# Performance work log

Measured on AMD Instinct MI355X. Metric: run time of the kernel, lower is better.

Reference implementation:

```python
import jax, jax.numpy as jnp
import numpy as np
from jax import lax

HID = 96              # hidden_dim (C)
DM  = 2 * HID         # SS2D d_model (real+imag interleaved channels)
DI  = 2 * DM          # d_inner (expand=2, VMamba default)
N   = 16              # d_state
K   = 4               # scan directions
R   = (DM + 15) // 16 # dt_rank = ceil(d_model/16)
B_, H_, W_ = 1, 64, 64


def _layernorm(x, w, b, eps=1e-5):
    m = x.mean(-1, keepdims=True)
    v = ((x - m) ** 2).mean(-1, keepdims=True)
    return (x - m) * lax.rsqrt(v + eps) * w + b


def _selective_scan(xs, delta, A, Bs, Cs):
    # xs, delta: (B,K,D,L); A: (K,D,N); Bs, Cs: (B,K,N,L)
    def step(h, inp):
        dt, Bt, Ct, ut = inp                              # (B,K,D),(B,K,N),(B,K,N),(B,K,D)
        dA = jnp.exp(dt[..., None] * A[None])             # (B,K,D,N)
        h = h * dA + dt[..., None] * Bt[:, :, None, :] * ut[..., None]
        y = jnp.einsum('bkdn,bkn->bkd', h, Ct)
        return h, y
    inputs = (jnp.moveaxis(delta, -1, 0), jnp.moveaxis(Bs, -1, 0),
              jnp.moveaxis(Cs, -1, 0), jnp.moveaxis(xs, -1, 0))
    h0 = jnp.zeros(xs.shape[:3] + (N,), xs.dtype)
    _, ys = lax.scan(step, h0, inputs)                    # (L,B,K,D)
    return jnp.moveaxis(ys, 0, -1)                        # (B,K,D,L)


def _forward_core(x, x_proj_w, dt_w, dt_b, A_logs, Ds):
    # x: (B, DI, H, W) -- 4-direction cross-scan (VMamba SS2D)
    B, D, H, W = x.shape
    L = H * W
    x_hw = x.reshape(B, D, L)
    x_wh = x.transpose(0, 1, 3, 2).reshape(B, D, L)
    x_hwwh = jnp.stack([x_hw, x_wh], axis=1)                    # (B,2,D,L)
    xs = jnp.concatenate([x_hwwh, jnp.flip(x_hwwh, -1)], 1)     # (B,4,D,L)
    x_dbl = jnp.einsum('bkdl,kcd->bkcl', xs, x_proj_w)          # (B,K,R+2N,L)
    dts, Bs, Cs = jnp.split(x_dbl, [R, R + N], axis=2)
    dts = jnp.einsum('bkrl,kdr->bkdl', dts, dt_w)
    delta = jax.nn.softplus(dts + dt_b[None, :, :, None])
    A = -jnp.exp(A_logs.reshape(K, D, N))
    ys = _selective_scan(xs, delta, A, Bs, Cs)
    out_y = ys + Ds.reshape(K, D)[None, :, :, None] * xs        # (B,4,D,L)
    inv_y = jnp.flip(out_y[:, 2:4], -1)
    tr = lambda t: t.reshape(B, D, W, H).transpose(0, 1, 3, 2).reshape(B, D, L)
    y = out_y[:, 0] + inv_y[:, 0] + tr(out_y[:, 1]) + tr(inv_y[:, 1])
    return y.transpose(0, 2, 1).reshape(B, H, W, D)


def _ss2d(x, in_proj_w, conv_w, conv_b, x_proj_w, dt_w, dt_b,
          A_logs, Ds, out_norm_w, out_norm_b, out_proj_w):
    # x: (B, H, Wf, DM)
    xz = x @ in_proj_w.T                                        # (B,H,Wf,2*DI)
    xc, z = jnp.split(xz, 2, axis=-1)
    xc = xc.transpose(0, 3, 1, 2)                               # (B,DI,H,Wf)
    xc = lax.conv_general_dilated(xc, conv_w, (1, 1), 'SAME',
                                  feature_group_count=DI,
                                  dimension_numbers=('NCHW', 'OIHW', 'NCHW'))
    xc = jax.nn.silu(xc + conv_b[None, :, None, None])
    y = _forward_core(xc, x_proj_w, dt_w, dt_b, A_logs, Ds)     # (B,H,Wf,DI)
    y = _layernorm(y, out_norm_w, out_norm_b)
    y = y * jax.nn.silu(z)
    return y @ out_proj_w.T                                     # (B,H,Wf,DM)


def _freq_vss(x, in_proj_w, conv_w, conv_b, x_proj_w, dt_w, dt_b,
              A_logs, Ds, out_norm_w, out_norm_b, out_proj_w):
    B, H, W, C = x.shape
    xf = jnp.fft.rfft2(x, axes=(1, 2), norm='ortho')            # (B,H,Wf,C) complex
    Wf = xf.shape[2]
    # interleave real/imag into channels: (B,H,Wf,C,2) -> (B,H,Wf,2C)
    x1 = jnp.stack([xf.real, xf.imag], axis=4).reshape(B, H, Wf, 2 * C)
    att = _ss2d(x1, in_proj_w, conv_w, conv_b, x_proj_w, dt_w, dt_b,
                A_logs, Ds, out_norm_w, out_norm_b, out_proj_w)
    att = att.reshape(B, H, Wf, C, 2)
    attc = lax.complex(att[..., 0], att[..., 1])
    x1r = jnp.fft.irfft2(attc, s=(H, W), axes=(1, 2), norm='ortho')
    return x + x1r                                              # residual (drop_path=0)


def setup_inputs() -> dict:
    key = jax.random.key(0)
    ks = jax.random.split(key, 8)
    s = 0.02
    return {
        'x': jax.random.normal(ks[0], (B_, H_, W_, HID), jnp.float32),
        'in_proj_w': jax.random.normal(ks[1], (2 * DI, DM), jnp.float32) * s,
        'conv_w': jax.random.normal(ks[2], (DI, 1, 3, 3), jnp.float32) * s,
        'conv_b': jnp.zeros((DI,), jnp.float32),
        'x_proj_w': jax.random.normal(ks[3], (K, R + 2 * N, DI), jnp.float32) * s,
        'dt_w': jax.random.normal(ks[4], (K, DI, R), jnp.float32) * s,
        'dt_b': jax.random.normal(ks[5], (K, DI), jnp.float32) * 0.1,
        'A_logs': jnp.tile(jnp.log(jnp.arange(1, N + 1, dtype=jnp.float32))[None], (K * DI, 1)),
        'Ds': jnp.ones((K * DI,), jnp.float32),
        'out_norm_w': jnp.ones((DI,), jnp.float32),
        'out_norm_b': jnp.zeros((DI,), jnp.float32),
        'out_proj_w': jax.random.normal(ks[6], (DM, DI), jnp.float32) * s,
    }


def reference(x, in_proj_w, conv_w, conv_b, x_proj_w, dt_w, dt_b,
              A_logs, Ds, out_norm_w, out_norm_b, out_proj_w):
    return _freq_vss(x, in_proj_w, conv_w, conv_b, x_proj_w, dt_w, dt_b,
                     A_logs, Ds, out_norm_w, out_norm_b, out_proj_w)
```

## Files before the change

kernel.cpp:

```cpp
#include <hip/hip_runtime.h>
#include <hip/hip_bf16.h>

#define LQ   2112
#define DQ   384
#define NST  16
#define HQ   64
#define WFQ  33
#define CQ   96
#define SC   66
#define KDN  24576

#define AIPW  0
#define ACW   147456
#define ACB   150912
#define AXPW  151296
#define ADTW  218880
#define ADTB  237312
#define AANEG 238848
#define ADS   263424
#define ANW   264960
#define ANB   265344
#define AOPW  265728
#define ARTOT 339456

#define OFF_FFT   339456
#define OFF_XZ    744960
#define OFF_XCV   2366976
#define OFF_G     3177984
#define OFF_SUMDT 3549696
#define OFF_HEND  3651072
#define OFF_YS    5273088
#define OFF_YS4   6084096

#define P_ZR  0
#define P_ZI  202752

static __device__ __forceinline__ float u2f(unsigned short u)
{ union { unsigned int i; float f; } v; v.i = ((unsigned int)u) << 16; return v.f; }

static __device__ __forceinline__ float ldin(const void* p, int o, int isbf)
{
    if (isbf) return u2f(((const unsigned short*)p)[o]);
    return ((const float*)p)[o];
}

static __device__ __forceinline__ int isbf_of(const void* ds)
{ return (((const unsigned int*)ds)[0] == 0x3F803F80u) ? 1 : 0; }

__global__ __launch_bounds__(256) void k_cvt_rfftw(
    const void* __restrict__ x,   const void* __restrict__ ipw,
    const void* __restrict__ cw,  const void* __restrict__ cb,
    const void* __restrict__ xpw, const void* __restrict__ dtw,
    const void* __restrict__ dtb, const void* __restrict__ alog,
    const void* __restrict__ ds,  const void* __restrict__ nw,
    const void* __restrict__ nb,  const void* __restrict__ opw,
    float* __restrict__ arena, float* __restrict__ Zr, float* __restrict__ Zi)
{
    const int isbf = isbf_of(ds);
    if (blockIdx.x < 1326) {
        int t = blockIdx.x * 256 + threadIdx.x;
        int o = t;
        if (o < 147456) { arena[t] = ldin(ipw, o, isbf); return; }  o -= 147456;
        if (o < 3456)   { arena[t] = ldin(cw, o, isbf);  return; }  o -= 3456;
        if (o < 384)    { arena[t] = ldin(cb, o, isbf);  return; }  o -= 384;
        if (o < 67584)  { arena[t] = ldin(xpw, o, isbf); return; }  o -= 67584;
        if (o < 18432)  { arena[t] = ldin(dtw, o, isbf); return; }  o -= 18432;
        if (o < 1536)   { arena[t] = ldin(dtb, o, isbf); return; }  o -= 1536;
        if (o < 24576)  { arena[t] = -expf(ldin(alog, o, isbf)); return; }  o -= 24576;
        if (o < 1536)   { arena[t] = ldin(ds, o, isbf);  return; }  o -= 1536;
        if (o < 384)    { arena[t] = ldin(nw, o, isbf);  return; }  o -= 384;
        if (o < 384)    { arena[t] = ldin(nb, o, isbf);  return; }  o -= 384;
        arena[t] = ldin(opw, o, isbf);
        return;
    }
    __shared__ float tc[64], ts[64];
    if (threadIdx.x < 64) {
        float ang = -6.283185307179586f * (float)threadIdx.x / 64.f;
        float s, c; __sincosf(ang, &s, &c); tc[threadIdx.x] = c; ts[threadIdx.x] = s;
    }
    __syncthreads();
    int tid = (blockIdx.x - 1326) * 256 + threadIdx.x;
    int c = tid % CQ; int f = (tid / CQ) % WFQ; int h = tid / (CQ * WFQ);
    const int base = h * 64 * CQ + c;
    float zr = 0.f, zi = 0.f; int j = 0;
#pragma unroll 4
    for (int w = 0; w < 64; w++) {
        float xv = ldin(x, base + w * CQ, isbf);
        zr += xv * tc[j]; zi += xv * ts[j];
        j += f; j &= 63;
    }
    Zr[tid] = zr; Zi[tid] = zi;
}

__global__ __launch_bounds__(256) void k_ffth(const float* __restrict__ Zr, const float* __restrict__ Zi,
                                              float* __restrict__ x1)
{
    __shared__ float tc[64], ts[64];
    if (threadIdx.x < 64) {
        float ang = -6.283185307179586f * (float)threadIdx.x / 64.f;
        float s, c; __sincosf(ang, &s, &c); tc[threadIdx.x] = c; ts[threadIdx.x] = s;
    }
    __syncthreads();
    int tid = blockIdx.x * 256 + threadIdx.x;
    int c = tid % CQ; int f = (tid / CQ) % WFQ; int u = tid / (CQ * WFQ);
    float xr = 0.f, xi = 0.f; int j = 0;
    int base = f * CQ + c;
#pragma unroll 4
    for (int h = 0; h < 64; h++) {
        float zr = Zr[base + h * (WFQ * CQ)];
        float zi = Zi[base + h * (WFQ * CQ)];
        xr += zr * tc[j] - zi * ts[j];
        xi += zr * ts[j] + zi * tc[j];
        j += u; j &= 63;
    }
    int l = u * WFQ + f;
    x1[l * 192 + 2 * c]     = xr * (1.f / 64.f);
    x1[l * 192 + 2 * c + 1] = xi * (1.f / 64.f);
}

typedef __attribute__((ext_vector_type(8))) __bf16 bf16x8;
typedef __attribute__((ext_vector_type(4))) float f32x4;

__global__ __launch_bounds__(256) void k_gemm(const float* __restrict__ A, const float* __restrict__ W,
                                              float* __restrict__ C, int N, int K, int sW, int sC)
{
    W += (size_t)blockIdx.z * sW; C += (size_t)blockIdx.z * sC;
    __shared__ __bf16 Asm[64 * 40];
    __shared__ __bf16 Bsm[64 * 40];
    const int tid = threadIdx.x;
    const int bm = blockIdx.y * 64, bn = blockIdx.x * 64;
    const int wv = tid >> 6, lane = tid & 63;
    const int srow = tid >> 2, skk = (tid & 3) * 8;
    const int fm = lane & 15, fq = lane >> 4;
    f32x4 acc0 = {0.f, 0.f, 0.f, 0.f}, acc1 = acc0, acc2 = acc0, acc3 = acc0;
    const __bf16* afp = Asm + (wv * 16 + fm) * 40 + fq * 8;
    const __bf16* bfp = Bsm + fm * 40 + fq * 8;
    for (int k0 = 0; k0 < K; k0 += 32) {
        {
            const float* ap = A + (size_t)(bm + srow) * K + k0 + skk;
            float4 a0 = *(const float4*)ap, a1 = *(const float4*)(ap + 4);
            bf16x8 v = { (__bf16)a0.x, (__bf16)a0.y, (__bf16)a0.z, (__bf16)a0.w,
                         (__bf16)a1.x, (__bf16)a1.y, (__bf16)a1.z, (__bf16)a1.w };
            *(bf16x8*)(Asm + srow * 40 + skk) = v;
        }
        {
            float4 b0 = {0.f,0.f,0.f,0.f}, b1 = b0;
            if (bn + srow < N) {
                const float* wp = W + (size_t)(bn + srow) * K + k0 + skk;
                b0 = *(const float4*)wp; b1 = *(const float4*)(wp + 4);
            }
            bf16x8 v = { (__bf16)b0.x, (__bf16)b0.y, (__bf16)b0.z, (__bf16)b0.w,
                         (__bf16)b1.x, (__bf16)b1.y, (__bf16)b1.z, (__bf16)b1.w };
            *(bf16x8*)(Bsm + srow * 40 + skk) = v;
        }
        __syncthreads();
        bf16x8 af = *(const bf16x8*)afp;
        bf16x8 fb0 = *(const bf16x8*)(bfp);
        bf16x8 fb1 = *(const bf16x8*)(bfp + 16 * 40);
        bf16x8 fb2 = *(const bf16x8*)(bfp + 32 * 40);
        bf16x8 fb3 = *(const bf16x8*)(bfp + 48 * 40);
        acc0 = __builtin_amdgcn_mfma_f32_16x16x32_bf16(af, fb0, acc0, 0, 0, 0);
        acc1 = __builtin_amdgcn_mfma_f32_16x16x32_bf16(af, fb1, acc1, 0, 0, 0);
        acc2 = __builtin_amdgcn_mfma_f32_16x16x32_bf16(af, fb2, acc2, 0, 0, 0);
        acc3 = __builtin_amdgcn_mfma_f32_16x16x32_bf16(af, fb3, acc3, 0, 0, 0);
        __syncthreads();
    }
    const int m0 = bm + wv * 16 + fq * 4;
#pragma unroll
    for (int nt = 0; nt < 4; nt++) {
        f32x4 a = (nt == 0) ? acc0 : ((nt == 1) ? acc1 : ((nt == 2) ? acc2 : acc3));
        int n = bn + nt * 16 + fm;
        if (n < N) {
#pragma unroll
            for (int r = 0; r < 4; r++)
                C[(size_t)(m0 + r) * N + n] = a[r];
        }
    }
}

__global__ __launch_bounds__(256) void k_conv(const float* __restrict__ xz,
                                              const float* __restrict__ ar,
                                              float* __restrict__ xcv)
{
    int tid = blockIdx.x * 256 + threadIdx.x;
    int d = tid % DQ; int lp = tid / DQ;
    int l0 = lp * 2;
    float w9[9];
#pragma unroll
    for (int i = 0; i < 9; i++) w9[i] = ar[ACW + d * 9 + i];
    float cb = ar[ACB + d];
#pragma unroll
    for (int q = 0; q < 2; q++) {
        int l = l0 + q;
        int h = l / WFQ; int f = l % WFQ;
        float acc = cb;
#pragma unroll
        for (int ky = 0; ky < 3; ky++) {
            int hh = h + ky - 1;
            if (hh < 0 || hh >= HQ) continue;
#pragma unroll
            for (int kx = 0; kx < 3; kx++) {
                int ff = f + kx - 1;
                if (ff < 0 || ff >= WFQ) continue;
                acc += w9[ky * 3 + kx] * xz[(size_t)(hh * WFQ + ff) * 768 + d];
            }
        }
        float sig = 1.f / (1.f + __expf(-acc));
        xcv[(size_t)l * DQ + d] = acc * sig;
    }
}

static __device__ __forceinline__ float softplus_f(float a)
{
    return (a > 15.f) ? a : __logf(1.f + __expf(a));
}

template<int KK> static __device__ __forceinline__ int chunk_l0(int s)
{
    if (KK == 0) return s * 32;
    if (KK == 1) return (s & 1) * 1056 + (s >> 1);
    if (KK == 2) return 2111 - s * 32;
    return 2111 - (s & 1) * 1056 - (s >> 1);
}
template<int KK> static __device__ __forceinline__ int chunk_stp()
{
    if (KK == 0) return 1;
    if (KK == 1) return 33;
    if (KK == 2) return -1;
    return -33;
}

template<int KK, int PASS2> static __device__ __forceinline__ void scan_body(
    const float* __restrict__ xcv, const float* __restrict__ G, const float* __restrict__ ar,
    float* __restrict__ hend, float* __restrict__ sumdt, float* __restrict__ ys4,
    float* __restrict__ dtL, float* __restrict__ duL,
    float* __restrict__ bvL, float* __restrict__ cvL)
{
    const int s = blockIdx.x, db = blockIdx.y;
    const int lane = threadIdx.x;
    const int d = lane & 15, ng = lane >> 4;
    const int stp = chunk_stp<KK>();
    const int l0 = chunk_l0<KK>(s);
    const float* Gk = G + (size_t)KK * (LQ * 44);

    {
        const int st = lane & 31;
        const int hi = lane >> 5;
        const int jb = hi * 8;
        const int lt = l0 + stp * st;
        const float* gr = Gk + lt * 44;
        float4 g0 = *(const float4*)(gr);
        float4 g1 = *(const float4*)(gr + 4);
        float4 g2 = *(const float4*)(gr + 8);
        float4 b0 = *(const float4*)(gr + 12 + jb);
        float4 b1 = *(const float4*)(gr + 16 + jb);
        *(float4*)(bvL + st * 20 + jb)     = b0;
        *(float4*)(bvL + st * 20 + jb + 4) = b1;
        if (PASS2) {
            float4 c0 = *(const float4*)(gr + 28 + jb);
            float4 c1 = *(const float4*)(gr + 32 + jb);
            *(float4*)(cvL + st * 20 + jb)     = c0;
            *(float4*)(cvL + st * 20 + jb + 4) = c1;
        }
        const float* ub = xcv + (size_t)lt * DQ + db * 16 + jb;
        float uu[8];
        *(float4*)(uu)     = *(const float4*)(ub);
        *(float4*)(uu + 4) = *(const float4*)(ub + 4);
#pragma unroll
        for (int j = 0; j < 8; j++) {
            const int kdj = KK * DQ + db * 16 + jb + j;
            const float* wp = ar + ADTW + kdj * 12;
            float acc = ar[ADTB + kdj]
                + wp[0] * g0.x + wp[1] * g0.y + wp[2]  * g0.z + wp[3]  * g0.w
                + wp[4] * g1.x + wp[5] * g1.y + wp[6]  * g1.z + wp[7]  * g1.w
                + wp[8] * g2.x + wp[9] * g2.y + wp[10] * g2.z + wp[11] * g2.w;
            float dtv = softplus_f(acc);
            dtL[st * 17 + jb + j] = dtv;
            duL[st * 17 + jb + j] = dtv * uu[j];
        }
    }
    __syncthreads();

    const int kd = KK * DQ + db * 16 + d;
    const int kdn = kd * NST + 4 * ng;
    const float4 Av = *(const float4*)(ar + AANEG + kdn);
    float h0 = 0.f, h1 = 0.f, h2 = 0.f, h3 = 0.f;
    if (PASS2) {
        float4 hh = *(const float4*)(hend + (size_t)s * KDN + kdn);
        h0 = hh.x; h1 = hh.y; h2 = hh.z; h3 = hh.w;
    }

    float sd_acc = 0.f;
#pragma unroll 8
    for (int i = 0; i < 32; i++) {
        float dt = dtL[i * 17 + d];
        float du = duL[i * 17 + d];
        float4 bv = *(const float4*)(bvL + i * 20 + 4 * ng);
        h0 = h0 * __expf(dt * Av.x) + du * bv.x;
        h1 = h1 * __expf(dt * Av.y) + du * bv.y;
        h2 = h2 * __expf(dt * Av.z) + du * bv.z;
        h3 = h3 * __expf(dt * Av.w) + du * bv.w;
        if (PASS2) {
            float4 cv = *(const float4*)(cvL + i * 20 + 4 * ng);
            float yp = h0 * cv.x + h1 * cv.y + h2 * cv.z + h3 * cv.w;
            yp += __shfl_xor(yp, 16);
            yp += __shfl_xor(yp, 32);
            if (ng == 0) duL[i * 17 + d] = yp;
        } else {
            sd_acc += dt;
        }
    }

    if (!PASS2) {
        *(float4*)(hend + (size_t)s * KDN + kdn) = make_float4(h0, h1, h2, h3);
        float sd = sd_acc;
        sd += __shfl_xor(sd, 16);
        sd += __shfl_xor(sd, 32);
        if (ng == 0) sumdt[s * 1536 + kd] = sd;
    } else {
        __syncthreads();
        float* ysk = ys4 + (size_t)KK * (LQ * DQ);
        const int sd16 = lane & 15, sg = lane >> 4;
#pragma unroll
        for (int e = 0; e < 8; e++) {
            const int step = e * 4 + sg;
            const int wl = l0 + stp * step;
            ysk[(size_t)wl * DQ + db * 16 + sd16] = duL[step * 17 + sd16];
        }
    }
}

__global__ __launch_bounds__(64, 4) void k_scan1(const float* __restrict__ xcv, const float* __restrict__ G,
                                                 const float* __restrict__ ar,
                                                 float* __restrict__ hend, float* __restrict__ sumdt,
                                                 float* __restrict__ ys4)
{
    __shared__ float smem[1728];
    float* dtL = smem; float* duL = smem + 544; float* bvL = smem + 1088;
    switch (blockIdx.z) {
        case 0: scan_body<0, 0>(xcv, G, ar, hend, sumdt, ys4, dtL, duL, bvL, nullptr); break;
        case 1: scan_body<1, 0>(xcv, G, ar, hend, sumdt, ys4, dtL, duL, bvL, nullptr); break;
        case 2: scan_body<2, 0>(xcv, G, ar, hend, sumdt, ys4, dtL, duL, bvL, nullptr); break;
        default: scan_body<3, 0>(xcv, G, ar, hend, sumdt, ys4, dtL, duL, bvL, nullptr); break;
    }
}

__global__ __launch_bounds__(64, 4) void k_scan2(const float* __restrict__ xcv, const float* __restrict__ G,
                                                 const float* __restrict__ ar,
                                                 float* __restrict__ hend, float* __restrict__ sumdt,
                                                 float* __restrict__ ys4)
{
    __shared__ float smem[2368];
    float* dtL = smem; float* duL = smem + 544; float* bvL = smem + 1088;
    float* cvL = smem + 1728;
    switch (blockIdx.z) {
        case 0: scan_body<0, 1>(xcv, G, ar, hend, sumdt, ys4, dtL, duL, bvL, cvL); break;
        case 1: scan_body<1, 1>(xcv, G, ar, hend, sumdt, ys4, dtL, duL, bvL, cvL); break;
        case 2: scan_body<2, 1>(xcv, G, ar, hend, sumdt, ys4, dtL, duL, bvL, cvL); break;
        default: scan_body<3, 1>(xcv, G, ar, hend, sumdt, ys4, dtL, duL, bvL, cvL); break;
    }
}

__global__ __launch_bounds__(256) void k_comb(const float* __restrict__ ar, const float* __restrict__ sumdt,
                                              float* __restrict__ hend)
{
    int tid = blockIdx.x * 256 + threadIdx.x;
    int kd = tid >> 4;
    float Av = ar[AANEG + tid];
    float hbuf[6], sbuf[6];
#pragma unroll
    for (int q = 0; q < 6; q++) {
        hbuf[q] = hend[(size_t)q * KDN + tid];
        sbuf[q] = sumdt[q * 1536 + kd];
    }
    float hp = 0.f;
    for (int s = 0; s < SC; s += 6) {
        float hc[6], sc6[6];
#pragma unroll
        for (int q = 0; q < 6; q++) { hc[q] = hbuf[q]; sc6[q] = sbuf[q]; }
#pragma unroll
        for (int q = 0; q < 6; q++) {
            int sn = s + 6 + q;
            if (sn < SC) {
                hbuf[q] = hend[(size_t)sn * KDN + tid];
                sbuf[q] = sumdt[sn * 1536 + kd];
            }
        }
#pragma unroll
        for (int q = 0; q < 6; q++) {
            hend[(size_t)(s + q) * KDN + tid] = hp;
            hp = hp * __expf(Av * sc6[q]) + hc[q];
        }
    }
}

__global__ __launch_bounds__(128) void k_lnmul(const float* __restrict__ ys4, const float* __restrict__ xcv,
                                               const float* __restrict__ xz, const float* __restrict__ ar,
                                               float* __restrict__ ym)
{
    int l = blockIdx.x; int tid = threadIdx.x;
    float v[3]; float s1 = 0.f, s2 = 0.f;
#pragma unroll
    for (int j = 0; j < 3; j++) {
        int d = tid + j * 128;
        size_t idx = (size_t)l * DQ + d;
        float sd = ar[ADS + d] + ar[ADS + DQ + d] + ar[ADS + 2 * DQ + d] + ar[ADS + 3 * DQ + d];
        float a = ys4[idx] + ys4[811008 + idx] + ys4[1622016 + idx] + ys4[2433024 + idx]
                + sd * xcv[idx];
        v[j] = a; s1 += a; s2 += a * a;
    }
#pragma unroll
    for (int off = 1; off < 64; off <<= 1) { s1 += __shfl_xor(s1, off); s2 += __shfl_xor(s2, off); }
    __shared__ float sh[4];
    if ((tid & 63) == 0) { sh[(tid >> 6) * 2] = s1; sh[(tid >> 6) * 2 + 1] = s2; }
    __syncthreads();
    s1 = sh[0] + sh[2]; s2 = sh[1] + sh[3];
    float m = s1 * (1.f / 384.f);
    float var = s2 * (1.f / 384.f) - m * m;
    float rs = rsqrtf(var + 1e-5f);
#pragma unroll
    for (int j = 0; j < 3; j++) {
        int d = tid + j * 128;
        float z = xz[(size_t)l * 768 + 384 + d];
        float sig = 1.f / (1.f + __expf(-z));
        ym[(size_t)l * DQ + d] = ((v[j] - m) * rs * ar[ANW + d] + ar[ANB + d]) * (z * sig);
    }
}

__global__ __launch_bounds__(256) void k_iffth(const float* __restrict__ att,
                                               float* __restrict__ Yr, float* __restrict__ Yi)
{
    __shared__ float tc[64], ts[64];
    if (threadIdx.x < 64) {
        float ang = 6.283185307179586f * (float)threadIdx.x / 64.f;
        float s, c; __sincosf(ang, &s, &c); tc[threadIdx.x] = c; ts[threadIdx.x] = s;
    }
    __syncthreads();
    int tid = blockIdx.x * 256 + threadIdx.x;
    int c = tid % CQ; int f = (tid / CQ) % WFQ; int hp = tid / (CQ * WFQ);
    float yr = 0.f, yi = 0.f; int j = 0;
#pragma unroll 4
    for (int h = 0; h < 64; h++) {
        const float* ap = att + (size_t)(h * WFQ + f) * 192 + 2 * c;
        float arv = ap[0], aiv = ap[1];
        yr += arv * tc[j] - aiv * ts[j];
        yi += arv * ts[j] + aiv * tc[j];
        j += hp; j &= 63;
    }
    Yr[tid] = yr * 0.125f;
    Yi[tid] = yi * 0.125f;
}

__global__ __launch_bounds__(256) void k_irfft_res(const float* __restrict__ Yr, const float* __restrict__ Yi,
                                                   const void* __restrict__ x, const void* __restrict__ ds,
                                                   void* __restrict__ out)
{
    __shared__ float tc[64], ts[64];
    if (threadIdx.x < 64) {
        float ang = 6.283185307179586f * (float)threadIdx.x / 64.f;
        float s, c; __sincosf(ang, &s, &c); tc[threadIdx.x] = c; ts[threadIdx.x] = s;
    }
    __syncthreads();
    const int isbf = isbf_of(ds);
    int tid = blockIdx.x * 256 + threadIdx.x;
    int c = tid % CQ; int w = (tid / CQ) % 64; int h = tid / (CQ * 64);
    const float* yr = Yr + h * (WFQ * CQ) + c;
    const float* yi = Yi + h * (WFQ * CQ) + c;
    float acc = yr[0];
    acc += ((w & 1) ? -1.f : 1.f) * yr[32 * CQ];
    float a2 = 0.f; int j = w & 63;
#pragma unroll 4
    for (int f = 1; f < 32; f++) {
        a2 += yr[f * CQ] * tc[j] - yi[f * CQ] * ts[j];
        j += w; j &= 63;
    }
    acc += 2.f * a2;
    float val = ldin(x, tid, isbf) + 0.125f * acc;
    if (isbf) ((__hip_bfloat16*)out)[tid] = __float2bfloat16(val);
    else      ((float*)out)[tid] = val;
}

extern "C" void kernel_launch(void* const* d_in, const int* in_sizes, int n_in,
                              void* d_out, int out_size, void* d_ws, size_t ws_size,
                              hipStream_t stream)
{
    float* ws    = (float*)d_ws;
    float* ar    = ws;
    float* Zr    = ws + OFF_FFT + P_ZR;
    float* Zi    = ws + OFF_FFT + P_ZI;
    float* xz    = ws + OFF_XZ;
    float* xcv   = ws + OFF_XCV;
    float* G     = ws + OFF_G;
    float* sumdt = ws + OFF_SUMDT;
    float* hend  = ws + OFF_HEND;
    float* x1    = ws + OFF_YS;
    float* ys4   = ws + OFF_YS4;

    float* ym   = hend;
    float* att  = xcv;

    k_cvt_rfftw<<<2118, 256, 0, stream>>>(d_in[0], d_in[1], d_in[2], d_in[3], d_in[4], d_in[5],
                                          d_in[6], d_in[7], d_in[8], d_in[9], d_in[10], d_in[11],
                                          ar, Zr, Zi);
    k_ffth<<<792, 256, 0, stream>>>(Zr, Zi, x1);
    k_gemm<<<dim3(12, 33, 1), 256, 0, stream>>>(x1, ar + AIPW, xz, 768, 192, 0, 0);
    k_conv<<<1584, 256, 0, stream>>>(xz, ar, xcv);
    k_gemm<<<dim3(1, 33, 4), 256, 0, stream>>>(xcv, ar + AXPW, G, 44, 384, 44 * 384, LQ * 44);
    k_scan1<<<dim3(SC, 24, 4), 64, 0, stream>>>(xcv, G, ar, hend, sumdt, ys4);
    k_comb<<<96, 256, 0, stream>>>(ar, sumdt, hend);
    k_scan2<<<dim3(SC, 24, 4), 64, 0, stream>>>(xcv, G, ar, hend, sumdt, ys4);
    k_lnmul<<<LQ, 128, 0, stream>>>(ys4, xcv, xz, ar, ym);
    k_gemm<<<dim3(3, 33, 1), 256, 0, stream>>>(ym, ar + AOPW, att, 192, 384, 0, 0);
    k_iffth<<<792, 256, 0, stream>>>(att, Zr, Zi);
    k_irfft_res<<<1536, 256, 0, stream>>>(Zr, Zi, d_in[0], d_in[8], d_out);
}
```

Before: 206.4 us.

## Give each scan thread one channel with all 16 states in registers

The chunked selective scan now maps one lane to one (direction, channel) and keeps all 16 state values in registers. This removes the shared-memory staging, barriers and cross-lane shuffle reductions. dt is computed per step inline, and the x_proj GEMM becomes a single launch with N=176 whose output interleaves the four directions per position. The cost is 4x fewer blocks (6 instead of 24 along y), more registers per thread, and serial per-step dependencies on global loads of G.

```diff
diff --git a/kernel.cpp b/kernel.cpp
--- a/kernel.cpp
+++ b/kernel.cpp
@@ -122,9 +122,8 @@
 typedef __attribute__((ext_vector_type(4))) float f32x4;
 
 __global__ __launch_bounds__(256) void k_gemm(const float* __restrict__ A, const float* __restrict__ W,
-                                              float* __restrict__ C, int N, int K, int sW, int sC)
-{
-    W += (size_t)blockIdx.z * sW; C += (size_t)blockIdx.z * sC;
+                                              float* __restrict__ C, int N, int K)
+{
     __shared__ __bf16 Asm[64 * 40];
     __shared__ __bf16 Bsm[64 * 40];
     const int tid = threadIdx.x;
@@ -232,132 +231,117 @@
 
 template<int KK, int PASS2> static __device__ __forceinline__ void scan_body(
     const float* __restrict__ xcv, const float* __restrict__ G, const float* __restrict__ ar,
-    float* __restrict__ hend, float* __restrict__ sumdt, float* __restrict__ ys4,
-    float* __restrict__ dtL, float* __restrict__ duL,
-    float* __restrict__ bvL, float* __restrict__ cvL)
+    float* __restrict__ hend, float* __restrict__ sumdt, float* __restrict__ ys4)
 {
     const int s = blockIdx.x, db = blockIdx.y;
     const int lane = threadIdx.x;
-    const int d = lane & 15, ng = lane >> 4;
     const int stp = chunk_stp<KK>();
     const int l0 = chunk_l0<KK>(s);
-    const float* Gk = G + (size_t)KK * (LQ * 44);
-
-    {
-        const int st = lane & 31;
-        const int hi = lane >> 5;
-        const int jb = hi * 8;
-        const int lt = l0 + stp * st;
-        const float* gr = Gk + lt * 44;
+    const int kd = KK * DQ + db * 64 + lane;
+
+    const float* wp = ar + ADTW + kd * 12;
+    const float4 wA = *(const float4*)(wp);
+    const float4 wB = *(const float4*)(wp + 4);
+    const float4 wC = *(const float4*)(wp + 8);
+    const float bias = ar[ADTB + kd];
+    const float* ap = ar + AANEG + kd * 16;
+    const float4 Av0 = *(const float4*)(ap);
+    const float4 Av1 = *(const float4*)(ap + 4);
+    const float4 Av2 = *(const float4*)(ap + 8);
+    const float4 Av3 = *(const float4*)(ap + 12);
+
+    float4 h0 = make_float4(0.f, 0.f, 0.f, 0.f), h1 = h0, h2 = h0, h3 = h0;
+    if (PASS2) {
+        const float* hp = hend + (size_t)s * KDN + kd * 16;
+        h0 = *(const float4*)(hp);
+        h1 = *(const float4*)(hp + 4);
+        h2 = *(const float4*)(hp + 8);
+        h3 = *(const float4*)(hp + 12);
+    }
+
+    float* ysk = ys4 + (size_t)KK * (LQ * DQ);
+    float sd_acc = 0.f;
+    for (int i = 0; i < 32; i++) {
+        const int lt = l0 + stp * i;
+        const float* gr = G + (size_t)lt * 176 + KK * 44;
         float4 g0 = *(const float4*)(gr);
         float4 g1 = *(const float4*)(gr + 4);
         float4 g2 = *(const float4*)(gr + 8);
-        float4 b0 = *(const float4*)(gr + 12 + jb);
-        float4 b1 = *(const float4*)(gr + 16 + jb);
-        *(float4*)(bvL + st * 20 + jb)     = b0;
-        *(float4*)(bvL + st * 20 + jb + 4) = b1;
+        float u = xcv[(size_t)lt * DQ + db * 64 + lane];
+        float acc = bias
+            + wA.x * g0.x + wA.y * g0.y + wA.z * g0.z + wA.w * g0.w
+            + wB.x * g1.x + wB.y * g1.y + wB.z * g1.z + wB.w * g1.w
+            + wC.x * g2.x + wC.y * g2.y + wC.z * g2.z + wC.w * g2.w;
+        float dt = softplus_f(acc);
+        float du = dt * u;
+        float4 b0 = *(const float4*)(gr + 12);
+        float4 b1 = *(const float4*)(gr + 16);
+        float4 b2 = *(const float4*)(gr + 20);
+        float4 b3 = *(const float4*)(gr + 24);
+        h0.x = h0.x * __expf(dt * Av0.x) + du * b0.x;
+        h0.y = h0.y * __expf(dt * Av0.y) + du * b0.y;
+        h0.z = h0.z * __expf(dt * Av0.z) + du * b0.z;
+        h0.w = h0.w * __expf(dt * Av0.w) + du * b0.w;
+        h1.x = h1.x * __expf(dt * Av1.x) + du * b1.x;
+        h1.y = h1.y * __expf(dt * Av1.y) + du * b1.y;
+        h1.z = h1.z * __expf(dt * Av1.z) + du * b1.z;
+        h1.w = h1.w * __expf(dt * Av1.w) + du * b1.w;
+        h2.x = h2.x * __expf(dt * Av2.x) + du * b2.x;
+        h2.y = h2.y * __expf(dt * Av2.y) + du * b2.y;
+        h2.z = h2.z * __expf(dt * Av2.z) + du * b2.z;
+        h2.w = h2.w * __expf(dt * Av2.w) + du * b2.w;
+        h3.x = h3.x * __expf(dt * Av3.x) + du * b3.x;
+        h3.y = h3.y * __expf(dt * Av3.y) + du * b3.y;
+        h3.z = h3.z * __expf(dt * Av3.z) + du * b3.z;
+        h3.w = h3.w * __expf(dt * Av3.w) + du * b3.w;
         if (PASS2) {
-            float4 c0 = *(const float4*)(gr + 28 + jb);
-            float4 c1 = *(const float4*)(gr + 32 + jb);
-            *(float4*)(cvL + st * 20 + jb)     = c0;
-            *(float4*)(cvL + st * 20 + jb + 4) = c1;
-        }
-        const float* ub = xcv + (size_t)lt * DQ + db * 16 + jb;
-        float uu[8];
-        *(float4*)(uu)     = *(const float4*)(ub);
-        *(float4*)(uu + 4) = *(const float4*)(ub + 4);
-#pragma unroll
-        for (int j = 0; j < 8; j++) {
-            const int kdj = KK * DQ + db * 16 + jb + j;
-            const float* wp = ar + ADTW + kdj * 12;
-            float acc = ar[ADTB + kdj]
-                + wp[0] * g0.x + wp[1] * g0.y + wp[2]  * g0.z + wp[3]  * g0.w
-                + wp[4] * g1.x + wp[5] * g1.y + wp[6]  * g1.z + wp[7]  * g1.w
-                + wp[8] * g2.x + wp[9] * g2.y + wp[10] * g2.z + wp[11] * g2.w;
-            float dtv = softplus_f(acc);
-            dtL[st * 17 + jb + j] = dtv;
-            duL[st * 17 + jb + j] = dtv * uu[j];
-        }
-    }
-    __syncthreads();
-
-    const int kd = KK * DQ + db * 16 + d;
-    const int kdn = kd * NST + 4 * ng;
-    const float4 Av = *(const float4*)(ar + AANEG + kdn);
-    float h0 = 0.f, h1 = 0.f, h2 = 0.f, h3 = 0.f;
-    if (PASS2) {
-        float4 hh = *(const float4*)(hend + (size_t)s * KDN + kdn);
-        h0 = hh.x; h1 = hh.y; h2 = hh.z; h3 = hh.w;
-    }
-
-    float sd_acc = 0.f;
-#pragma unroll 8
-    for (int i = 0; i < 32; i++) {
-        float dt = dtL[i * 17 + d];
-        float du = duL[i * 17 + d];
-        float4 bv = *(const float4*)(bvL + i * 20 + 4 * ng);
-        h0 = h0 * __expf(dt * Av.x) + du * bv.x;
-        h1 = h1 * __expf(dt * Av.y) + du * bv.y;
-        h2 = h2 * __expf(dt * Av.z) + du * bv.z;
-        h3 = h3 * __expf(dt * Av.w) + du * bv.w;
-        if (PASS2) {
-            float4 cv = *(const float4*)(cvL + i * 20 + 4 * ng);
-            float yp = h0 * cv.x + h1 * cv.y + h2 * cv.z + h3 * cv.w;
-            yp += __shfl_xor(yp, 16);
-            yp += __shfl_xor(yp, 32);
-            if (ng == 0) duL[i * 17 + d] = yp;
+            float4 c0 = *(const float4*)(gr + 28);
+            float4 c1 = *(const float4*)(gr + 32);
+            float4 c2 = *(const float4*)(gr + 36);
+            float4 c3 = *(const float4*)(gr + 40);
+            float y0 = h0.x * c0.x + h0.y * c0.y + h0.z * c0.z + h0.w * c0.w;
+            float y1 = h1.x * c1.x + h1.y * c1.y + h1.z * c1.z + h1.w * c1.w;
+            float y2 = h2.x * c2.x + h2.y * c2.y + h2.z * c2.z + h2.w * c2.w;
+            float y3 = h3.x * c3.x + h3.y * c3.y + h3.z * c3.z + h3.w * c3.w;
+            ysk[(size_t)lt * DQ + db * 64 + lane] = (y0 + y1) + (y2 + y3);
         } else {
             sd_acc += dt;
         }
     }
 
     if (!PASS2) {
-        *(float4*)(hend + (size_t)s * KDN + kdn) = make_float4(h0, h1, h2, h3);
-        float sd = sd_acc;
-        sd += __shfl_xor(sd, 16);
-        sd += __shfl_xor(sd, 32);
-        if (ng == 0) sumdt[s * 1536 + kd] = sd;
-    } else {
-        __syncthreads();
-        float* ysk = ys4 + (size_t)KK * (LQ * DQ);
-        const int sd16 = lane & 15, sg = lane >> 4;
-#pragma unroll
-        for (int e = 0; e < 8; e++) {
-            const int step = e * 4 + sg;
-            const int wl = l0 + stp * step;
-            ysk[(size_t)wl * DQ + db * 16 + sd16] = duL[step * 17 + sd16];
-        }
-    }
-}
-
-__global__ __launch_bounds__(64, 4) void k_scan1(const float* __restrict__ xcv, const float* __restrict__ G,
-                                                 const float* __restrict__ ar,
-                                                 float* __restrict__ hend, float* __restrict__ sumdt,
-                                                 float* __restrict__ ys4)
-{
-    __shared__ float smem[1728];
-    float* dtL = smem; float* duL = smem + 544; float* bvL = smem + 1088;
+        float* hp = hend + (size_t)s * KDN + kd * 16;
+        *(float4*)(hp)      = h0;
+        *(float4*)(hp + 4)  = h1;
+        *(float4*)(hp + 8)  = h2;
+        *(float4*)(hp + 12) = h3;
+        sumdt[s * 1536 + kd] = sd_acc;
+    }
+}
+
+__global__ __launch_bounds__(64) void k_scan1(const float* __restrict__ xcv, const float* __restrict__ G,
+                                              const float* __restrict__ ar,
+                                              float* __restrict__ hend, float* __restrict__ sumdt,
+                                              float* __restrict__ ys4)
+{
     switch (blockIdx.z) {
-        case 0: scan_body<0, 0>(xcv, G, ar, hend, sumdt, ys4, dtL, duL, bvL, nullptr); break;
-        case 1: scan_body<1, 0>(xcv, G, ar, hend, sumdt, ys4, dtL, duL, bvL, nullptr); break;
-        case 2: scan_body<2, 0>(xcv, G, ar, hend, sumdt, ys4, dtL, duL, bvL, nullptr); break;
-        default: scan_body<3, 0>(xcv, G, ar, hend, sumdt, ys4, dtL, duL, bvL, nullptr); break;
-    }
-}
-
-__global__ __launch_bounds__(64, 4) void k_scan2(const float* __restrict__ xcv, const float* __restrict__ G,
-                                                 const float* __restrict__ ar,
-                                                 float* __restrict__ hend, float* __restrict__ sumdt,
-                                                 float* __restrict__ ys4)
-{
-    __shared__ float smem[2368];
-    float* dtL = smem; float* duL = smem + 544; float* bvL = smem + 1088;
-    float* cvL = smem + 1728;
+        case 0: scan_body<0, 0>(xcv, G, ar, hend, sumdt, ys4); break;
+        case 1: scan_body<1, 0>(xcv, G, ar, hend, sumdt, ys4); break;
+        case 2: scan_body<2, 0>(xcv, G, ar, hend, sumdt, ys4); break;
+        default: scan_body<3, 0>(xcv, G, ar, hend, sumdt, ys4); break;
+    }
+}
+
+__global__ __launch_bounds__(64) void k_scan2(const float* __restrict__ xcv, const float* __restrict__ G,
+                                              const float* __restrict__ ar,
+                                              float* __restrict__ hend, float* __restrict__ sumdt,
+                                              float* __restrict__ ys4)
+{
     switch (blockIdx.z) {
-        case 0: scan_body<0, 1>(xcv, G, ar, hend, sumdt, ys4, dtL, duL, bvL, cvL); break;
-        case 1: scan_body<1, 1>(xcv, G, ar, hend, sumdt, ys4, dtL, duL, bvL, cvL); break;
-        case 2: scan_body<2, 1>(xcv, G, ar, hend, sumdt, ys4, dtL, duL, bvL, cvL); break;
-        default: scan_body<3, 1>(xcv, G, ar, hend, sumdt, ys4, dtL, duL, bvL, cvL); break;
+        case 0: scan_body<0, 1>(xcv, G, ar, hend, sumdt, ys4); break;
+        case 1: scan_body<1, 1>(xcv, G, ar, hend, sumdt, ys4); break;
+        case 2: scan_body<2, 1>(xcv, G, ar, hend, sumdt, ys4); break;
+        default: scan_body<3, 1>(xcv, G, ar, hend, sumdt, ys4); break;
     }
 }
 
@@ -503,14 +487,14 @@
                                           d_in[6], d_in[7], d_in[8], d_in[9], d_in[10], d_in[11],
                                           ar, Zr, Zi);
     k_ffth<<<792, 256, 0, stream>>>(Zr, Zi, x1);
-    k_gemm<<<dim3(12, 33, 1), 256, 0, stream>>>(x1, ar + AIPW, xz, 768, 192, 0, 0);
+    k_gemm<<<dim3(12, 33), 256, 0, stream>>>(x1, ar + AIPW, xz, 768, 192);
     k_conv<<<1584, 256, 0, stream>>>(xz, ar, xcv);
-    k_gemm<<<dim3(1, 33, 4), 256, 0, stream>>>(xcv, ar + AXPW, G, 44, 384, 44 * 384, LQ * 44);
-    k_scan1<<<dim3(SC, 24, 4), 64, 0, stream>>>(xcv, G, ar, hend, sumdt, ys4);
+    k_gemm<<<dim3(3, 33), 256, 0, stream>>>(xcv, ar + AXPW, G, 176, 384);
+    k_scan1<<<dim3(SC, 6, 4), 64, 0, stream>>>(xcv, G, ar, hend, sumdt, ys4);
     k_comb<<<96, 256, 0, stream>>>(ar, sumdt, hend);
-    k_scan2<<<dim3(SC, 24, 4), 64, 0, stream>>>(xcv, G, ar, hend, sumdt, ys4);
+    k_scan2<<<dim3(SC, 6, 4), 64, 0, stream>>>(xcv, G, ar, hend, sumdt, ys4);
     k_lnmul<<<LQ, 128, 0, stream>>>(ys4, xcv, xz, ar, ym);
-    k_gemm<<<dim3(3, 33, 1), 256, 0, stream>>>(ym, ar + AOPW, att, 192, 384, 0, 0);
+    k_gemm<<<dim3(3, 33), 256, 0, stream>>>(ym, ar + AOPW, att, 192, 384);
     k_iffth<<<792, 256, 0, stream>>>(att, Zr, Zi);
     k_irfft_res<<<1536, 256, 0, stream>>>(Zr, Zi, d_in[0], d_in[8], d_out);
 }
```

New measurement: 211.1 us. 2.3% more time.
